# Kernel tuning notes

Measured on AMD Instinct MI355X. Metric: run time of the kernel, lower is better.

## Reference

```python
import jax, jax.numpy as jnp
import numpy as np

B, S, D = 4, 2048, 1024
HEADS, KEY_SIZE, SIZE_PER_HEAD = 16, 64, 64
OUT_DIM = HEADS * SIZE_PER_HEAD
NEG_BIG = 1e10


def setup_inputs() -> dict:
    key = jax.random.key(0)
    ks = jax.random.split(key, 6)
    q_value = jax.random.normal(ks[0], (B, S, D), dtype=jnp.float32)
    k_value = jax.random.normal(ks[1], (B, S, D), dtype=jnp.float32)
    v_value = jax.random.normal(ks[2], (B, S, D), dtype=jnp.float32)
    v_mask = jnp.ones((B, S, 1), dtype=jnp.float32)
    q_mask = jnp.ones((B, S, 1), dtype=jnp.float32)
    scale = 1.0 / np.sqrt(D)
    Wq = jax.random.normal(ks[3], (D, HEADS * KEY_SIZE), dtype=jnp.float32) * scale
    Wk = jax.random.normal(ks[4], (D, HEADS * KEY_SIZE), dtype=jnp.float32) * scale
    Wv = jax.random.normal(ks[5], (D, OUT_DIM), dtype=jnp.float32) * scale
    return {"q_value": q_value, "k_value": k_value, "v_value": v_value,
            "v_mask": v_mask, "q_mask": q_mask, "Wq": Wq, "Wk": Wk, "Wv": Wv}


def reference(q_value, k_value, v_value, v_mask, q_mask, Wq, Wk, Wv):
    b, sq, _ = q_value.shape
    sk = k_value.shape[1]
    # projections (no bias) -> [B, S, H, dh]
    qw = (q_value @ Wq).reshape(b, sq, HEADS, KEY_SIZE)
    kw = (k_value @ Wk).reshape(b, sk, HEADS, KEY_SIZE)
    vw = (v_value @ Wv).reshape(b, sk, HEADS, SIZE_PER_HEAD)
    # scores [B, H, Sq, Sk], scaled by sqrt(key_size)
    scores = jnp.einsum('bqhd,bkhd->bhqk', qw, kw) / jnp.sqrt(
        jnp.asarray(KEY_SIZE, dtype=qw.dtype))
    # additive key-side mask: v_mask [B, Sk, 1] -> broadcast over heads/queries
    scores = scores - (1.0 - v_mask[:, None, None, :, 0]) * NEG_BIG
    attn = jax.nn.softmax(scores, axis=-1)
    out = jnp.einsum('bhqk,bkhd->bqhd', attn, vw).reshape(b, sq, OUT_DIM)
    # multiplicative query-side mask
    return out * q_mask
```

## Files before the change

### kernel.cpp

```cpp
#include <hip/hip_runtime.h>

typedef __bf16 bf16_t;
typedef __bf16 bf16x8 __attribute__((ext_vector_type(8)));
typedef __bf16 bf16x4 __attribute__((ext_vector_type(4)));
typedef float  f32x4  __attribute__((ext_vector_type(4)));

#define MFMA16(A, B, C) __builtin_amdgcn_mfma_f32_16x16x32_bf16((A), (B), (C), 0, 0, 0)

constexpr int BB = 4;
constexpr int SS = 2048;
constexpr int DD = 1024;
constexpr int HH = 16;
constexpr int DH = 64;
constexpr float C1 = 0.18033688011112042f;

__device__ __forceinline__ void async_copy16(const void* g, void* l) {
    __builtin_amdgcn_global_load_lds(
        (const __attribute__((address_space(1))) void*)g,
        (__attribute__((address_space(3))) void*)l, 16, 0, 0);
}

__global__ __launch_bounds__(256) void conv_kernel(
    const float* __restrict__ q, const float* __restrict__ k,
    const float* __restrict__ v, bf16_t* __restrict__ outb)
{
    const float* src = blockIdx.z == 0 ? q : blockIdx.z == 1 ? k : v;
    bf16_t* dst = outb + ((size_t)blockIdx.z << 23);
    size_t i = ((size_t)blockIdx.x * 256 + threadIdx.x) * 8;
    f32x4 a = *(const f32x4*)&src[i];
    f32x4 b = *(const f32x4*)&src[i + 4];
    bf16x8 o;
    o[0] = (bf16_t)a[0]; o[1] = (bf16_t)a[1]; o[2] = (bf16_t)a[2]; o[3] = (bf16_t)a[3];
    o[4] = (bf16_t)b[0]; o[5] = (bf16_t)b[1]; o[6] = (bf16_t)b[2]; o[7] = (bf16_t)b[3];
    *(bf16x8*)&dst[i] = o;
}

__global__ __launch_bounds__(256) void wtrans_kernel(
    const float* __restrict__ Wq, const float* __restrict__ Wk,
    const float* __restrict__ Wv, bf16_t* __restrict__ Wt)
{
    const float* W = blockIdx.z == 0 ? Wq : blockIdx.z == 1 ? Wk : Wv;
    bf16_t* T = Wt + ((size_t)blockIdx.z << 20);

    __shared__ __align__(16) bf16_t tile[64][72];

    const int k0 = blockIdx.x * 64;
    const int n0 = blockIdx.y * 64;
    const int tid = threadIdx.x;

    #pragma unroll
    for (int i = 0; i < 4; i++) {
        int idx = tid + i * 256;
        int kk = idx >> 4;
        int nn = (idx & 15) * 4;
        f32x4 w = *(const f32x4*)&W[(size_t)(k0 + kk) * 1024 + n0 + nn];
        tile[nn + 0][kk] = (bf16_t)w[0];
        tile[nn + 1][kk] = (bf16_t)w[1];
        tile[nn + 2][kk] = (bf16_t)w[2];
        tile[nn + 3][kk] = (bf16_t)w[3];
    }
    __syncthreads();
    #pragma unroll
    for (int i = 0; i < 2; i++) {
        int idx = tid + i * 256;
        int nn = idx >> 3;
        int kk = (idx & 7) * 8;
        *(bf16x8*)&T[(size_t)(n0 + nn) * 1024 + k0 + kk] =
            *(const bf16x8*)&tile[nn][kk];
    }
}

__global__ __launch_bounds__(256) void proj_kernel(
    const bf16_t* __restrict__ Ab, const bf16_t* __restrict__ Wt,
    bf16_t* __restrict__ qw, bf16_t* __restrict__ kw, bf16_t* __restrict__ vwt)
{
    const int which = blockIdx.z;
    const bf16_t* A = Ab + ((size_t)which << 23);
    const bf16_t* T = Wt + ((size_t)which << 20);

    __shared__ bf16_t Alds[128 * 64];
    __shared__ bf16_t Blds[128 * 64];

    const int tid = threadIdx.x;
    const int lane = tid & 63;
    const int wave = tid >> 6;
    const int quad = lane >> 4;
    const int l16 = lane & 15;

    const int id = blockIdx.x;
    const int xg = id & 7;
    const int sl = id >> 3;
    const int m0 = (((xg << 3) | (sl >> 3))) * 128;
    const int n0 = (sl & 7) * 128;

    const int wm = (wave >> 1) * 64;
    const int wn = (wave & 1) * 64;

    const int srow = lane >> 3;
    const int schk = lane & 7;

    f32x4 zero4 = {0.f, 0.f, 0.f, 0.f};
    f32x4 acc[4][4];
    #pragma unroll
    for (int i = 0; i < 4; i++)
        #pragma unroll
        for (int j = 0; j < 4; j++) acc[i][j] = zero4;

    for (int k0 = 0; k0 < DD; k0 += 64) {
        #pragma unroll
        for (int j = 0; j < 4; j++) {
            int r0 = wave * 32 + j * 8;
            int row = r0 + srow;
            int c = schk ^ (row & 7);
            async_copy16(&A[(size_t)(m0 + row) * 1024 + k0 + c * 8], &Alds[r0 * 64]);
        }
        #pragma unroll
        for (int j = 0; j < 4; j++) {
            int r0 = wave * 32 + j * 8;
            int row = r0 + srow;
            int c = schk ^ (row & 7);
            async_copy16(&T[(size_t)(n0 + row) * 1024 + k0 + c * 8], &Blds[r0 * 64]);
        }
        __syncthreads();

        #pragma unroll
        for (int s = 0; s < 2; s++) {
            bf16x8 af[4], bfr[4];
            #pragma unroll
            for (int mi = 0; mi < 4; mi++)
                af[mi] = *(const bf16x8*)&Alds[(wm + mi * 16 + l16) * 64 +
                             (((s * 4 + quad) ^ (l16 & 7)) << 3)];
            #pragma unroll
            for (int ni = 0; ni < 4; ni++)
                bfr[ni] = *(const bf16x8*)&Blds[(wn + ni * 16 + l16) * 64 +
                              (((s * 4 + quad) ^ (l16 & 7)) << 3)];
            #pragma unroll
            for (int mi = 0; mi < 4; mi++)
                #pragma unroll
                for (int ni = 0; ni < 4; ni++)
                    acc[mi][ni] = MFMA16(af[mi], bfr[ni], acc[mi][ni]);
        }
        __syncthreads();
    }

    if (which < 2) {
        bf16_t* Cout = which == 0 ? qw : kw;
        #pragma unroll
        for (int mi = 0; mi < 4; mi++)
            #pragma unroll
            for (int ni = 0; ni < 4; ni++)
                #pragma unroll
                for (int r = 0; r < 4; r++) {
                    int row = m0 + wm + mi * 16 + quad * 4 + r;
                    int col = n0 + wn + ni * 16 + l16;
                    Cout[(size_t)row * 1024 + col] = (bf16_t)acc[mi][ni][r];
                }
    } else {
        #pragma unroll
        for (int mi = 0; mi < 4; mi++)
            #pragma unroll
            for (int ni = 0; ni < 4; ni++) {
                int s0 = m0 + wm + mi * 16 + quad * 4;
                int col = n0 + wn + ni * 16 + l16;
                int b = s0 >> 11, s = s0 & 2047;
                int h = col >> 6, d = col & 63;
                bf16x4 p;
                p[0] = (bf16_t)acc[mi][ni][0]; p[1] = (bf16_t)acc[mi][ni][1];
                p[2] = (bf16_t)acc[mi][ni][2]; p[3] = (bf16_t)acc[mi][ni][3];
                *(bf16x4*)&vwt[(((size_t)((b * HH + h) * DH + d)) << 11) + s] = p;
            }
    }
}

__global__ __launch_bounds__(256) void attn_kernel(
    const bf16_t* __restrict__ qw, const bf16_t* __restrict__ kw,
    const bf16_t* __restrict__ vwt, const float* __restrict__ v_mask,
    const float* __restrict__ q_mask, float* __restrict__ out)
{
    const int linear = blockIdx.x;
    const int xg = linear & 7;
    const int sl = linear >> 3;
    const int grp = (xg << 3) | (sl >> 4);
    const int qt = sl & 15;
    const int b = grp >> 4;
    const int h = grp & 15;

    __shared__ bf16_t Klds[128 * 64];
    __shared__ bf16_t Vtlds[64 * 128];
    __shared__ float vml[128];

    const int tid = threadIdx.x;
    const int lane = tid & 63;
    const int wave = tid >> 6;
    const int quad = lane >> 4;
    const int l16 = lane & 15;

    const int q0 = qt * 128 + wave * 32;
    bf16_t* Pw = &Klds[wave * 2048];

    bf16x8 bq[2][2];
    #pragma unroll
    for (int qi = 0; qi < 2; qi++)
        #pragma unroll
        for (int dk = 0; dk < 2; dk++) {
            int q = q0 + qi * 16 + l16;
            int d = dk * 32 + quad * 8;
            bq[qi][dk] = *(const bf16x8*)&qw[(size_t)(b * SS + q) * 1024 + h * 64 + d];
        }

    float l_i[2] = {0.f, 0.f};
    f32x4 zero4 = {0.f, 0.f, 0.f, 0.f};
    f32x4 oacc[4][2];
    #pragma unroll
    for (int dt = 0; dt < 4; dt++) { oacc[dt][0] = zero4; oacc[dt][1] = zero4; }

    const int kp = lane & 7, kro = lane >> 3;
    const int vp = lane & 15, vro = lane >> 4;

    for (int kt = 0; kt < SS; kt += 128) {
        #pragma unroll
        for (int j = 0; j < 4; j++) {
            int r0 = wave * 32 + j * 8;
            int row = r0 + kro;
            int c = kp ^ (row & 7);
            async_copy16(&kw[(size_t)(b * SS + kt + row) * 1024 + h * 64 + c * 8],
                         &Klds[r0 * 64]);
        }
        #pragma unroll
        for (int j = 0; j < 4; j++) {
            int r0 = wave * 16 + j * 4;
            int row = r0 + vro;
            int c = vp ^ (row & 15);
            async_copy16(&vwt[(((size_t)((b * HH + h) * DH + row)) << 11) + kt + c * 8],
                         &Vtlds[r0 * 128]);
        }
        if (tid < 128)
            vml[tid] = (1.0f - v_mask[b * SS + kt + tid]) * 1.4426950408889634e10f;
        __syncthreads();

        f32x4 st[8][2];
        #pragma unroll
        for (int ki = 0; ki < 8; ki++) { st[ki][0] = zero4; st[ki][1] = zero4; }
        #pragma unroll
        for (int ki = 0; ki < 8; ki++) {
            int base = (ki * 16 + l16) * 64;
            bf16x8 ak0 = *(const bf16x8*)&Klds[base + ((quad ^ (l16 & 7)) << 3)];
            bf16x8 ak1 = *(const bf16x8*)&Klds[base + (((4 + quad) ^ (l16 & 7)) << 3)];
            #pragma unroll
            for (int qi = 0; qi < 2; qi++) {
                st[ki][qi] = MFMA16(ak0, bq[qi][0], st[ki][qi]);
                st[ki][qi] = MFMA16(ak1, bq[qi][1], st[ki][qi]);
            }
        }
        #pragma unroll
        for (int ki = 0; ki < 8; ki++) {
            f32x4 vm4 = *(const f32x4*)&vml[ki * 16 + quad * 4];
            #pragma unroll
            for (int qi = 0; qi < 2; qi++)
                #pragma unroll
                for (int r = 0; r < 4; r++) {
                    float p = __builtin_amdgcn_exp2f(
                        __builtin_fmaf(st[ki][qi][r], C1, -vm4[r]));
                    st[ki][qi][r] = p;
                    l_i[qi] += p;
                }
        }
        __syncthreads();

        #pragma unroll
        for (int half = 0; half < 2; half++) {
            #pragma unroll
            for (int qi = 0; qi < 2; qi++)
                #pragma unroll
                for (int kj = 0; kj < 4; kj++) {
                    int ki = half * 4 + kj;
                    bf16x4 p4;
                    p4[0] = (bf16_t)st[ki][qi][0]; p4[1] = (bf16_t)st[ki][qi][1];
                    p4[2] = (bf16_t)st[ki][qi][2]; p4[3] = (bf16_t)st[ki][qi][3];
                    int c = 2 * kj + (quad >> 1);
                    *(bf16x4*)&Pw[(qi * 16 + l16) * 64 +
                                  ((c ^ (l16 & 7)) << 3) + (quad & 1) * 4] = p4;
                }
            asm volatile("" ::: "memory");
            #pragma unroll
            for (int ks = 0; ks < 2; ks++) {
                bf16x8 bp[2];
                #pragma unroll
                for (int qi = 0; qi < 2; qi++)
                    bp[qi] = *(const bf16x8*)&Pw[(qi * 16 + l16) * 64 +
                                 (((ks * 4 + quad) ^ (l16 & 7)) << 3)];
                #pragma unroll
                for (int dt = 0; dt < 4; dt++) {
                    int rowv = dt * 16 + l16;
                    bf16x8 av = *(const bf16x8*)&Vtlds[rowv * 128 +
                                 ((((half * 2 + ks) * 4 + quad) ^ l16) << 3)];
                    #pragma unroll
                    for (int qi = 0; qi < 2; qi++)
                        oacc[dt][qi] = MFMA16(av, bp[qi], oacc[dt][qi]);
                }
            }
            asm volatile("" ::: "memory");
        }
        __syncthreads();
    }

    #pragma unroll
    for (int qi = 0; qi < 2; qi++) {
        l_i[qi] += __shfl_xor(l_i[qi], 16);
        l_i[qi] += __shfl_xor(l_i[qi], 32);
    }

    #pragma unroll
    for (int qi = 0; qi < 2; qi++) {
        int q = q0 + qi * 16 + l16;
        float sc = q_mask[b * SS + q] / l_i[qi];
        #pragma unroll
        for (int dt = 0; dt < 4; dt++) {
            int d = dt * 16 + quad * 4;
            f32x4 o;
            o[0] = oacc[dt][qi][0] * sc; o[1] = oacc[dt][qi][1] * sc;
            o[2] = oacc[dt][qi][2] * sc; o[3] = oacc[dt][qi][3] * sc;
            *(f32x4*)&out[(size_t)(b * SS + q) * 1024 + h * 64 + d] = o;
        }
    }
}

extern "C" void kernel_launch(void* const* d_in, const int* in_sizes, int n_in,
                              void* d_out, int out_size, void* d_ws, size_t ws_size,
                              hipStream_t stream)
{
    const float* q  = (const float*)d_in[0];
    const float* k  = (const float*)d_in[1];
    const float* v  = (const float*)d_in[2];
    const float* vm = (const float*)d_in[3];
    const float* qm = (const float*)d_in[4];
    const float* Wq = (const float*)d_in[5];
    const float* Wk = (const float*)d_in[6];
    const float* Wv = (const float*)d_in[7];
    float* out = (float*)d_out;

    const size_t elems = (size_t)BB * SS * DD;
    bf16_t* Ab  = (bf16_t*)d_ws;
    bf16_t* qw  = Ab + 3 * elems;
    bf16_t* kw  = qw + elems;
    bf16_t* vwt = kw + elems;
    bf16_t* Wt  = vwt + elems;

    conv_kernel<<<dim3(4096, 1, 3), 256, 0, stream>>>(q, k, v, Ab);
    wtrans_kernel<<<dim3(16, 16, 3), 256, 0, stream>>>(Wq, Wk, Wv, Wt);
    proj_kernel<<<dim3(512, 1, 3), 256, 0, stream>>>(Ab, Wt, qw, kw, vwt);
    attn_kernel<<<dim3(1024, 1, 1), 256, 0, stream>>>(qw, kw, vwt, vm, qm, out);
}
```

Baseline: 320.2 us.

## Switch attention to 32x32 MFMA with register P reuse and double-buffered K/V tiles

Rewrites the attention inner loop to use 32x32x16 bf16 MFMA tiles over 64-key blocks. The probability matrix is packed to bf16 and rearranged across lanes with permlane32_swap, so it feeds the PV MFMA straight from registers instead of a round trip through LDS. K/V tiles are double-buffered, with the next tile's async load issued before the current tile is computed, leaving one barrier per iteration. This removes LDS traffic and barriers, at the cost of more accumulator registers and dependence on the permlane32_swap intrinsic and its lane layout being correct.

```diff
diff --git a/kernel.cpp b/kernel.cpp
--- a/kernel.cpp
+++ b/kernel.cpp
@@ -3,9 +3,14 @@
 typedef __bf16 bf16_t;
 typedef __bf16 bf16x8 __attribute__((ext_vector_type(8)));
 typedef __bf16 bf16x4 __attribute__((ext_vector_type(4)));
+typedef __bf16 bf16x2 __attribute__((ext_vector_type(2)));
 typedef float  f32x4  __attribute__((ext_vector_type(4)));
+typedef float  f32x16 __attribute__((ext_vector_type(16)));
+typedef unsigned int u32x4 __attribute__((ext_vector_type(4)));
+typedef int i32x2 __attribute__((ext_vector_type(2)));
 
 #define MFMA16(A, B, C) __builtin_amdgcn_mfma_f32_16x16x32_bf16((A), (B), (C), 0, 0, 0)
+#define MFMA32(A, B, C) __builtin_amdgcn_mfma_f32_32x32x16_bf16((A), (B), (C), 0, 0, 0)
 
 constexpr int BB = 4;
 constexpr int SS = 2048;
@@ -18,6 +23,19 @@
     __builtin_amdgcn_global_load_lds(
         (const __attribute__((address_space(1))) void*)g,
         (__attribute__((address_space(3))) void*)l, 16, 0, 0);
+}
+
+__device__ __forceinline__ unsigned pack_bf16(float lo, float hi) {
+    bf16x2 t;
+    t[0] = (bf16_t)lo;
+    t[1] = (bf16_t)hi;
+    return __builtin_bit_cast(unsigned, t);
+}
+
+__device__ __forceinline__ void permswap(unsigned& a, unsigned& b) {
+    i32x2 r = __builtin_amdgcn_permlane32_swap((int)a, (int)b, false, false);
+    a = (unsigned)r[0];
+    b = (unsigned)r[1];
 }
 
 __global__ __launch_bounds__(256) void conv_kernel(
@@ -185,142 +203,132 @@
     const int b = grp >> 4;
     const int h = grp & 15;
 
-    __shared__ bf16_t Klds[128 * 64];
-    __shared__ bf16_t Vtlds[64 * 128];
-    __shared__ float vml[128];
+    __shared__ __align__(16) bf16_t Klds[2][64 * 64];
+    __shared__ __align__(16) bf16_t Vtlds[2][64 * 64];
+    __shared__ float vml[2][64];
 
     const int tid = threadIdx.x;
     const int lane = tid & 63;
     const int wave = tid >> 6;
-    const int quad = lane >> 4;
-    const int l16 = lane & 15;
-
+    const int l5 = lane & 31;
+    const int hi = lane >> 5;
     const int q0 = qt * 128 + wave * 32;
-    bf16_t* Pw = &Klds[wave * 2048];
-
-    bf16x8 bq[2][2];
-    #pragma unroll
-    for (int qi = 0; qi < 2; qi++)
-        #pragma unroll
-        for (int dk = 0; dk < 2; dk++) {
-            int q = q0 + qi * 16 + l16;
-            int d = dk * 32 + quad * 8;
-            bq[qi][dk] = *(const bf16x8*)&qw[(size_t)(b * SS + q) * 1024 + h * 64 + d];
-        }
-
-    float l_i[2] = {0.f, 0.f};
-    f32x4 zero4 = {0.f, 0.f, 0.f, 0.f};
-    f32x4 oacc[4][2];
-    #pragma unroll
-    for (int dt = 0; dt < 4; dt++) { oacc[dt][0] = zero4; oacc[dt][1] = zero4; }
-
-    const int kp = lane & 7, kro = lane >> 3;
-    const int vp = lane & 15, vro = lane >> 4;
-
-    for (int kt = 0; kt < SS; kt += 128) {
-        #pragma unroll
-        for (int j = 0; j < 4; j++) {
-            int r0 = wave * 32 + j * 8;
-            int row = r0 + kro;
-            int c = kp ^ (row & 7);
+
+    const int srow = lane >> 3;
+    const int schk = lane & 7;
+
+    bf16x8 qf[4];
+    #pragma unroll
+    for (int c = 0; c < 4; ++c)
+        qf[c] = *(const bf16x8*)&qw[(size_t)(b * SS + q0 + l5) * 1024 + h * 64 +
+                                    c * 16 + hi * 8];
+
+    f32x16 zero16;
+    #pragma unroll
+    for (int i = 0; i < 16; ++i) zero16[i] = 0.f;
+
+    auto stage = [&](int bi, int kt) {
+        #pragma unroll
+        for (int j = 0; j < 2; ++j) {
+            int r0 = (wave * 2 + j) * 8;
+            int row = r0 + srow;
+            int c = schk ^ (row & 7);
             async_copy16(&kw[(size_t)(b * SS + kt + row) * 1024 + h * 64 + c * 8],
-                         &Klds[r0 * 64]);
-        }
-        #pragma unroll
-        for (int j = 0; j < 4; j++) {
-            int r0 = wave * 16 + j * 4;
-            int row = r0 + vro;
-            int c = vp ^ (row & 15);
-            async_copy16(&vwt[(((size_t)((b * HH + h) * DH + row)) << 11) + kt + c * 8],
-                         &Vtlds[r0 * 128]);
-        }
-        if (tid < 128)
-            vml[tid] = (1.0f - v_mask[b * SS + kt + tid]) * 1.4426950408889634e10f;
-        __syncthreads();
-
-        f32x4 st[8][2];
-        #pragma unroll
-        for (int ki = 0; ki < 8; ki++) { st[ki][0] = zero4; st[ki][1] = zero4; }
-        #pragma unroll
-        for (int ki = 0; ki < 8; ki++) {
-            int base = (ki * 16 + l16) * 64;
-            bf16x8 ak0 = *(const bf16x8*)&Klds[base + ((quad ^ (l16 & 7)) << 3)];
-            bf16x8 ak1 = *(const bf16x8*)&Klds[base + (((4 + quad) ^ (l16 & 7)) << 3)];
-            #pragma unroll
-            for (int qi = 0; qi < 2; qi++) {
-                st[ki][qi] = MFMA16(ak0, bq[qi][0], st[ki][qi]);
-                st[ki][qi] = MFMA16(ak1, bq[qi][1], st[ki][qi]);
-            }
-        }
-        #pragma unroll
-        for (int ki = 0; ki < 8; ki++) {
-            f32x4 vm4 = *(const f32x4*)&vml[ki * 16 + quad * 4];
-            #pragma unroll
-            for (int qi = 0; qi < 2; qi++)
+                         &Klds[bi][r0 * 64]);
+        }
+        #pragma unroll
+        for (int j = 0; j < 2; ++j) {
+            int r0 = (wave * 2 + j) * 8;
+            int d = r0 + srow;
+            int c = schk ^ (d & 7);
+            async_copy16(&vwt[(((size_t)((b * HH + h) * DH + d)) << 11) + kt + c * 8],
+                         &Vtlds[bi][r0 * 64]);
+        }
+        if (tid < 64)
+            vml[bi][tid] = (1.0f - v_mask[b * SS + kt + tid]) * 1.4426950408889634e10f;
+    };
+
+    stage(0, 0);
+    __syncthreads();
+
+    f32x16 o0 = zero16, o1 = zero16;
+    f32x4 l4 = {0.f, 0.f, 0.f, 0.f};
+
+    for (int t = 0; t < 32; ++t) {
+        const int cur = t & 1;
+        if (t < 31) stage(cur ^ 1, (t + 1) * 64);
+
+        f32x16 st0 = zero16, st1 = zero16;
+        #pragma unroll
+        for (int c = 0; c < 4; ++c) {
+            const int sw = ((c * 2 + hi) ^ (l5 & 7)) << 3;
+            bf16x8 k0 = *(const bf16x8*)&Klds[cur][l5 * 64 + sw];
+            bf16x8 k1 = *(const bf16x8*)&Klds[cur][(32 + l5) * 64 + sw];
+            st0 = MFMA32(k0, qf[c], st0);
+            st1 = MFMA32(k1, qf[c], st1);
+        }
+
+        #pragma unroll
+        for (int kb = 0; kb < 2; ++kb) {
+            f32x16 st = kb ? st1 : st0;
+            #pragma unroll
+            for (int g = 0; g < 4; ++g) {
+                f32x4 vm4 = *(const f32x4*)&vml[cur][kb * 32 + g * 8 + hi * 4];
                 #pragma unroll
-                for (int r = 0; r < 4; r++) {
+                for (int j = 0; j < 4; ++j) {
                     float p = __builtin_amdgcn_exp2f(
-                        __builtin_fmaf(st[ki][qi][r], C1, -vm4[r]));
-                    st[ki][qi][r] = p;
-                    l_i[qi] += p;
-                }
-        }
-        __syncthreads();
-
-        #pragma unroll
-        for (int half = 0; half < 2; half++) {
-            #pragma unroll
-            for (int qi = 0; qi < 2; qi++)
-                #pragma unroll
-                for (int kj = 0; kj < 4; kj++) {
-                    int ki = half * 4 + kj;
-                    bf16x4 p4;
-                    p4[0] = (bf16_t)st[ki][qi][0]; p4[1] = (bf16_t)st[ki][qi][1];
-                    p4[2] = (bf16_t)st[ki][qi][2]; p4[3] = (bf16_t)st[ki][qi][3];
-                    int c = 2 * kj + (quad >> 1);
-                    *(bf16x4*)&Pw[(qi * 16 + l16) * 64 +
-                                  ((c ^ (l16 & 7)) << 3) + (quad & 1) * 4] = p4;
-                }
-            asm volatile("" ::: "memory");
-            #pragma unroll
-            for (int ks = 0; ks < 2; ks++) {
-                bf16x8 bp[2];
-                #pragma unroll
-                for (int qi = 0; qi < 2; qi++)
-                    bp[qi] = *(const bf16x8*)&Pw[(qi * 16 + l16) * 64 +
-                                 (((ks * 4 + quad) ^ (l16 & 7)) << 3)];
-                #pragma unroll
-                for (int dt = 0; dt < 4; dt++) {
-                    int rowv = dt * 16 + l16;
-                    bf16x8 av = *(const bf16x8*)&Vtlds[rowv * 128 +
-                                 ((((half * 2 + ks) * 4 + quad) ^ l16) << 3)];
-                    #pragma unroll
-                    for (int qi = 0; qi < 2; qi++)
-                        oacc[dt][qi] = MFMA16(av, bp[qi], oacc[dt][qi]);
+                        __builtin_fmaf(st[g * 4 + j], C1, -vm4[j]));
+                    st[g * 4 + j] = p;
+                    l4[j] += p;
                 }
             }
-            asm volatile("" ::: "memory");
-        }
-        __syncthreads();
-    }
-
-    #pragma unroll
-    for (int qi = 0; qi < 2; qi++) {
-        l_i[qi] += __shfl_xor(l_i[qi], 16);
-        l_i[qi] += __shfl_xor(l_i[qi], 32);
-    }
-
-    #pragma unroll
-    for (int qi = 0; qi < 2; qi++) {
-        int q = q0 + qi * 16 + l16;
-        float sc = q_mask[b * SS + q] / l_i[qi];
-        #pragma unroll
-        for (int dt = 0; dt < 4; dt++) {
-            int d = dt * 16 + quad * 4;
-            f32x4 o;
-            o[0] = oacc[dt][qi][0] * sc; o[1] = oacc[dt][qi][1] * sc;
-            o[2] = oacc[dt][qi][2] * sc; o[3] = oacc[dt][qi][3] * sc;
-            *(f32x4*)&out[(size_t)(b * SS + q) * 1024 + h * 64 + d] = o;
+            unsigned a0 = pack_bf16(st[0],  st[1]);
+            unsigned a1 = pack_bf16(st[2],  st[3]);
+            unsigned a2 = pack_bf16(st[4],  st[5]);
+            unsigned a3 = pack_bf16(st[6],  st[7]);
+            unsigned a4 = pack_bf16(st[8],  st[9]);
+            unsigned a5 = pack_bf16(st[10], st[11]);
+            unsigned a6 = pack_bf16(st[12], st[13]);
+            unsigned a7 = pack_bf16(st[14], st[15]);
+            permswap(a0, a2);
+            permswap(a1, a3);
+            permswap(a4, a6);
+            permswap(a5, a7);
+            u32x4 w0 = {a0, a1, a2, a3};
+            u32x4 w1 = {a4, a5, a6, a7};
+            bf16x8 bp0 = __builtin_bit_cast(bf16x8, w0);
+            bf16x8 bp1 = __builtin_bit_cast(bf16x8, w1);
+
+            #pragma unroll
+            for (int c = 0; c < 2; ++c) {
+                bf16x8 bp = c ? bp1 : bp0;
+                const int sw = (((kb * 4 + c * 2 + hi)) ^ (l5 & 7)) << 3;
+                bf16x8 av0 = *(const bf16x8*)&Vtlds[cur][l5 * 64 + sw];
+                bf16x8 av1 = *(const bf16x8*)&Vtlds[cur][(32 + l5) * 64 + sw];
+                o0 = MFMA32(av0, bp, o0);
+                o1 = MFMA32(av1, bp, o1);
+            }
+        }
+        if (t < 31) __syncthreads();
+    }
+
+    float l_i = (l4[0] + l4[1]) + (l4[2] + l4[3]);
+    l_i += __shfl_xor(l_i, 32);
+
+    const int q = q0 + l5;
+    const float sc = q_mask[b * SS + q] / l_i;
+    #pragma unroll
+    for (int db = 0; db < 2; ++db) {
+        const f32x16 oa = db ? o1 : o0;
+        #pragma unroll
+        for (int g = 0; g < 4; ++g) {
+            f32x4 o4;
+            o4[0] = oa[g * 4 + 0] * sc;
+            o4[1] = oa[g * 4 + 1] * sc;
+            o4[2] = oa[g * 4 + 2] * sc;
+            o4[3] = oa[g * 4 + 3] * sc;
+            *(f32x4*)&out[(size_t)(b * SS + q) * 1024 + h * 64 +
+                          db * 32 + g * 8 + hi * 4] = o4;
         }
     }
 }
```

Measured after the change: 318.9 us. Within noise of the previous version (-0.4%).
